# Performance work log

Measured on AMD Instinct MI355X. Metric: run time of the kernel, lower is better.

The kernel has to match this reference:

```python
import jax, jax.numpy as jnp
import numpy as np


def setup_inputs() -> dict:
    key = jax.random.key(0)
    k_x, k_w, k_b = jax.random.split(key, 3)
    B, Cin, H, W = 32, 256, 56, 56
    Cout, KH, KW = 256, 3, 3
    x = jax.random.normal(k_x, (B, Cin, H, W), dtype=jnp.float32)
    fp_weight = jax.random.normal(k_w, (Cout, Cin, KH, KW), dtype=jnp.float32)
    # binary quantization, conv_mode='input_ch': per-output-channel scale
    scaling_factors = jnp.mean(jnp.abs(fp_weight), axis=(1, 2, 3), keepdims=True)  # [Cout,1,1,1]
    quant_weights = jnp.sign(fp_weight)  # values in {-1,0,1}
    bias = jax.random.normal(k_b, (Cout,), dtype=jnp.float32)
    return {"x": x, "scaling_factors": scaling_factors,
            "quant_weights": quant_weights, "bias": bias}


def reference(x, scaling_factors, quant_weights, bias):
    # Dequantize: per-out-channel scale times sign weights
    new_weights = scaling_factors * quant_weights  # [Cout,Cin,3,3]
    out = jax.lax.conv_general_dilated(
        x, new_weights,
        window_strides=(1, 1),
        padding=((1, 1), (1, 1)),
        dimension_numbers=("NCHW", "OIHW", "NCHW"),
    )
    return out + bias[None, :, None, None]
```

## Files before the change

kernel.cpp:

```cpp
#include <hip/hip_runtime.h>

using half8   = __attribute__((ext_vector_type(8))) _Float16;
using floatx4 = __attribute__((ext_vector_type(4))) float;
using floatx2 = __attribute__((ext_vector_type(2))) float;
using short8  = __attribute__((ext_vector_type(8))) short;

__global__ void repack_weights(const float* __restrict__ qw,
                               _Float16* __restrict__ wre, int n) {
  int t = blockIdx.x * 256 + threadIdx.x;
  if (t >= n) return;
  int c = t & 255, co = (t >> 8) & 255, s = t >> 16;
  wre[t] = (_Float16)qw[(co * 256 + c) * 9 + s];
}

__global__ __launch_bounds__(512, 4) void binconv_fused(
    const float* __restrict__ x, const float* __restrict__ scale,
    const float* __restrict__ bias, const _Float16* __restrict__ wre,
    float* __restrict__ out)
{
  __shared__ _Float16 xs[2 * 4 * 64 * 40];

  const int tid  = threadIdx.x;
  const int nb   = blockIdx.x;
  const int b    = nb / 28;
  const int h0   = (nb % 28) * 2;
  const int wave = tid >> 6;
  const int lane = tid & 63;
  const int nl   = lane & 15;
  const int quad = lane >> 4;
  const int co_wave = wave * 32;

  {
    short8 z = {0, 0, 0, 0, 0, 0, 0, 0};
    short8* xs8 = reinterpret_cast<short8*>(xs);
#pragma unroll
    for (int i = 0; i < 5; ++i) xs8[tid + i * 512] = z;
  }

  const int r     = wave >> 1;
  const int chalf = wave & 1;
  const int sc    = lane & 15;
  const int q     = lane >> 4;
  const int ch    = chalf * 16 + sc;
  const int w0    = q * 14;
  const int h     = h0 + r - 1;
  const bool hok  = (h >= 0) && (h < 56);
  const float* xc = x + (((size_t)b * 256 + ch) * 56 + (hok ? h : 0)) * 56 + w0;
  _Float16* const wrow = xs + r * 2560 + ch;

  floatx2 va[7];

  int bbase[7];
#pragma unroll
  for (int j = 0; j < 7; ++j) {
    int n = j * 16 + nl;
    int rr = (n >= 56) ? 1 : 0;
    int w = n - rr * 56;
    bbase[j] = (rr * 64 + w) * 80 + quad * 16;
  }

  const _Float16* aptr[2];
#pragma unroll
  for (int mi = 0; mi < 2; ++mi)
    aptr[mi] = wre + (co_wave + mi * 16 + nl) * 256 + quad * 8;

  floatx4 acc[2][7];
#pragma unroll
  for (int mi = 0; mi < 2; ++mi)
#pragma unroll
    for (int j = 0; j < 7; ++j)
      acc[mi][j] = (floatx4){0.f, 0.f, 0.f, 0.f};

  __syncthreads();

  if (hok) {
#pragma unroll
    for (int i = 0; i < 7; ++i)
      va[i] = *reinterpret_cast<const floatx2*>(xc + 2 * i);
#pragma unroll
    for (int i = 0; i < 7; ++i) {
      wrow[(w0 + 2 * i + 1) * 40] = (_Float16)va[i][0];
      wrow[(w0 + 2 * i + 2) * 40] = (_Float16)va[i][1];
    }
  }

  int bufe = 0;
  for (int cc = 0; cc < 8; ++cc) {
    __syncthreads();
    if (cc < 7 && hok) {
      const float* A = xc + (size_t)(cc + 1) * 100352;
#pragma unroll
      for (int i = 0; i < 7; ++i)
        va[i] = *reinterpret_cast<const floatx2*>(A + 2 * i);
    }
    const int c0 = cc * 32;
    const char* xb = reinterpret_cast<const char*>(xs) + bufe * 2;
    __builtin_amdgcn_s_setprio(1);
#pragma unroll
    for (int s = 0; s < 9; ++s) {
      const int kh = s / 3, kw = s - kh * 3;
      half8 a[2];
#pragma unroll
      for (int mi = 0; mi < 2; ++mi)
        a[mi] = *reinterpret_cast<const half8*>(aptr[mi] + s * 65536 + c0);
      const int soff = (kh * 64 + kw) * 80;
#pragma unroll
      for (int j = 0; j < 7; ++j) {
        half8 bf = *reinterpret_cast<const half8*>(xb + bbase[j] + soff);
#pragma unroll
        for (int mi = 0; mi < 2; ++mi)
          acc[mi][j] = __builtin_amdgcn_mfma_f32_16x16x32_f16(a[mi], bf, acc[mi][j], 0, 0, 0);
      }
    }
    __builtin_amdgcn_s_setprio(0);
    if (cc < 7 && hok) {
      _Float16* d = wrow + (bufe ^ 10240);
#pragma unroll
      for (int i = 0; i < 7; ++i) {
        d[(w0 + 2 * i + 1) * 40] = (_Float16)va[i][0];
        d[(w0 + 2 * i + 2) * 40] = (_Float16)va[i][1];
      }
    }
    bufe ^= 10240;
  }

#pragma unroll
  for (int mi = 0; mi < 2; ++mi) {
#pragma unroll
    for (int reg = 0; reg < 4; ++reg) {
      int co = co_wave + mi * 16 + quad * 4 + reg;
      float s_ = scale[co];
      float bi = bias[co];
#pragma unroll
      for (int j = 0; j < 7; ++j) {
        int n = j * 16 + nl;
        int rr = (n >= 56) ? 1 : 0;
        int w = n - rr * 56;
        out[(((size_t)b * 256 + co) * 56 + (h0 + rr)) * 56 + w] =
            acc[mi][j][reg] * s_ + bi;
      }
    }
  }
}

extern "C" void kernel_launch(void* const* d_in, const int* in_sizes, int n_in,
                              void* d_out, int out_size, void* d_ws, size_t ws_size,
                              hipStream_t stream) {
  const float* x     = (const float*)d_in[0];
  const float* scale = (const float*)d_in[1];
  const float* qw    = (const float*)d_in[2];
  const float* bias  = (const float*)d_in[3];
  float* out = (float*)d_out;

  _Float16* wre = (_Float16*)d_ws;

  repack_weights<<<2304, 256, 0, stream>>>(qw, wre, 9 * 256 * 256);
  binconv_fused<<<896, 512, 0, stream>>>(x, scale, bias, wre, out);
}
```

Baseline: 323.0 us.

## Pre-transpose input to padded fp16 layout and stream it into LDS with direct loads

```diff
diff --git a/kernel.cpp b/kernel.cpp
--- a/kernel.cpp
+++ b/kernel.cpp
@@ -4,6 +4,155 @@
 using floatx4 = __attribute__((ext_vector_type(4))) float;
 using floatx2 = __attribute__((ext_vector_type(2))) float;
 using short8  = __attribute__((ext_vector_type(8))) short;
+
+#define XT_ROW_ELEMS 2560
+#define XT_ROW_BYTES 5120
+#define XT_OFF ((size_t)2 << 20)
+#define XT_BYTES ((size_t)256 * 58 * XT_ROW_BYTES)
+
+__device__ __forceinline__ void dma16(const void* g, void* l) {
+  __builtin_amdgcn_global_load_lds(
+      (const __attribute__((address_space(1))) void*)g,
+      (__attribute__((address_space(3))) void*)l, 16, 0, 0);
+}
+
+__global__ __launch_bounds__(256) void prep_kernel(
+    const float* __restrict__ x, const float* __restrict__ qw,
+    _Float16* __restrict__ wre, _Float16* __restrict__ xt)
+{
+  const int bid = blockIdx.x;
+  const int t = threadIdx.x;
+  if (bid >= 14848) {
+    int idx = (bid - 14848) * 256 + t;
+    int c = idx & 255, co = (idx >> 8) & 255, s = idx >> 16;
+    wre[idx] = (_Float16)qw[(co * 256 + c) * 9 + s];
+    return;
+  }
+  __shared__ _Float16 lt[32 * 57];
+  const int hh = bid % 58;
+  const int bc = bid / 58;
+  const int cc = bc & 7, b = bc >> 3;
+  _Float16* dst = xt + ((size_t)bc * 58 + hh) * XT_ROW_ELEMS;
+  const bool interior = (hh >= 1) && (hh <= 56);
+  if (interior) {
+    const int c = t >> 3, j = t & 7;
+    const float* src = x + (((size_t)(b * 256 + cc * 32 + c)) * 56 + (hh - 1)) * 56 + j * 7;
+#pragma unroll
+    for (int i = 0; i < 7; ++i) lt[c * 57 + j * 7 + i] = (_Float16)src[i];
+  }
+  __syncthreads();
+  for (int ch = t; ch < 320; ch += 256) {
+    int pos = ch / 5, sl = ch - pos * 5;
+    short8 v = {0, 0, 0, 0, 0, 0, 0, 0};
+    if (interior && sl < 4 && pos >= 1 && pos <= 56) {
+      int w = pos - 1;
+#pragma unroll
+      for (int i = 0; i < 8; ++i)
+        v[i] = __builtin_bit_cast(short, lt[(sl * 8 + i) * 57 + w]);
+    }
+    *reinterpret_cast<short8*>(dst + ch * 8) = v;
+  }
+}
+
+__global__ __launch_bounds__(256, 4) void binconv_v3(
+    const float* __restrict__ scale, const float* __restrict__ bias,
+    const _Float16* __restrict__ wre, const _Float16* __restrict__ xt,
+    float* __restrict__ out)
+{
+  __shared__ _Float16 xs[2 * 4 * 64 * 40];
+
+  const int tid    = threadIdx.x;
+  const int bid    = blockIdx.x;
+  const int cohalf = bid & 1;
+  const int nb     = bid >> 1;
+  const int b      = nb / 28;
+  const int h0     = (nb % 28) * 2;
+  const int wave   = tid >> 6;
+  const int lane   = tid & 63;
+  const int nl     = lane & 15;
+  const int quad   = lane >> 4;
+  const int co_wave = cohalf * 128 + wave * 32;
+
+  int bbase[7];
+#pragma unroll
+  for (int j = 0; j < 7; ++j) {
+    int n = j * 16 + nl;
+    int r = (n >= 56) ? 1 : 0;
+    int w = n - r * 56;
+    bbase[j] = (r * 64 + w) * 80 + quad * 16;
+  }
+
+  const _Float16* aptr[2];
+#pragma unroll
+  for (int mi = 0; mi < 2; ++mi)
+    aptr[mi] = wre + (co_wave + mi * 16 + nl) * 256 + quad * 8;
+
+  floatx4 acc[2][7];
+#pragma unroll
+  for (int mi = 0; mi < 2; ++mi)
+#pragma unroll
+    for (int j = 0; j < 7; ++j)
+      acc[mi][j] = (floatx4){0.f, 0.f, 0.f, 0.f};
+
+  const char* xsrc = (const char*)(xt + ((size_t)(b * 8) * 58 + h0) * XT_ROW_ELEMS);
+  const int wlane = wave * XT_ROW_BYTES + lane * 16;
+  const int wldso = wave * XT_ROW_BYTES;
+
+#pragma unroll
+  for (int i = 0; i < 5; ++i)
+    dma16(xsrc + wlane + i * 1024, (char*)xs + wldso + i * 1024);
+
+  int bufoff = 0;
+  for (int cc = 0; cc < 8; ++cc) {
+    __syncthreads();
+    if (cc < 7) {
+      const char* srcn = xsrc + (size_t)(cc + 1) * (58 * XT_ROW_BYTES);
+#pragma unroll
+      for (int i = 0; i < 5; ++i)
+        dma16(srcn + wlane + i * 1024,
+              (char*)xs + (bufoff ^ 20480) + wldso + i * 1024);
+    }
+    const int c0 = cc * 32;
+    const char* xb = (const char*)xs + bufoff;
+    __builtin_amdgcn_s_setprio(1);
+#pragma unroll
+    for (int s = 0; s < 9; ++s) {
+      const int kh = s / 3, kw = s - kh * 3;
+      half8 a[2];
+#pragma unroll
+      for (int mi = 0; mi < 2; ++mi)
+        a[mi] = *reinterpret_cast<const half8*>(aptr[mi] + s * 65536 + c0);
+      const int soff = (kh * 64 + kw) * 80;
+#pragma unroll
+      for (int j = 0; j < 7; ++j) {
+        half8 bf = *reinterpret_cast<const half8*>(xb + bbase[j] + soff);
+#pragma unroll
+        for (int mi = 0; mi < 2; ++mi)
+          acc[mi][j] = __builtin_amdgcn_mfma_f32_16x16x32_f16(a[mi], bf, acc[mi][j], 0, 0, 0);
+      }
+    }
+    __builtin_amdgcn_s_setprio(0);
+    bufoff ^= 20480;
+  }
+
+#pragma unroll
+  for (int mi = 0; mi < 2; ++mi) {
+#pragma unroll
+    for (int reg = 0; reg < 4; ++reg) {
+      int co = co_wave + mi * 16 + quad * 4 + reg;
+      float s_ = scale[co];
+      float bi = bias[co];
+#pragma unroll
+      for (int j = 0; j < 7; ++j) {
+        int n = j * 16 + nl;
+        int r = (n >= 56) ? 1 : 0;
+        int w = n - r * 56;
+        out[(((size_t)b * 256 + co) * 56 + (h0 + r)) * 56 + w] =
+            acc[mi][j][reg] * s_ + bi;
+      }
+    }
+  }
+}
 
 __global__ void repack_weights(const float* __restrict__ qw,
                                _Float16* __restrict__ wre, int n) {
@@ -19,7 +168,6 @@
     float* __restrict__ out)
 {
   __shared__ _Float16 xs[2 * 4 * 64 * 40];
-
   const int tid  = threadIdx.x;
   const int nb   = blockIdx.x;
   const int b    = nb / 28;
@@ -29,14 +177,12 @@
   const int nl   = lane & 15;
   const int quad = lane >> 4;
   const int co_wave = wave * 32;
-
   {
     short8 z = {0, 0, 0, 0, 0, 0, 0, 0};
     short8* xs8 = reinterpret_cast<short8*>(xs);
 #pragma unroll
     for (int i = 0; i < 5; ++i) xs8[tid + i * 512] = z;
   }
-
   const int r     = wave >> 1;
   const int chalf = wave & 1;
   const int sc    = lane & 15;
@@ -47,9 +193,7 @@
   const bool hok  = (h >= 0) && (h < 56);
   const float* xc = x + (((size_t)b * 256 + ch) * 56 + (hok ? h : 0)) * 56 + w0;
   _Float16* const wrow = xs + r * 2560 + ch;
-
   floatx2 va[7];
-
   int bbase[7];
 #pragma unroll
   for (int j = 0; j < 7; ++j) {
@@ -58,21 +202,17 @@
     int w = n - rr * 56;
     bbase[j] = (rr * 64 + w) * 80 + quad * 16;
   }
-
   const _Float16* aptr[2];
 #pragma unroll
   for (int mi = 0; mi < 2; ++mi)
     aptr[mi] = wre + (co_wave + mi * 16 + nl) * 256 + quad * 8;
-
   floatx4 acc[2][7];
 #pragma unroll
   for (int mi = 0; mi < 2; ++mi)
 #pragma unroll
     for (int j = 0; j < 7; ++j)
       acc[mi][j] = (floatx4){0.f, 0.f, 0.f, 0.f};
-
   __syncthreads();
-
   if (hok) {
 #pragma unroll
     for (int i = 0; i < 7; ++i)
@@ -83,7 +223,6 @@
       wrow[(w0 + 2 * i + 2) * 40] = (_Float16)va[i][1];
     }
   }
-
   int bufe = 0;
   for (int cc = 0; cc < 8; ++cc) {
     __syncthreads();
@@ -95,7 +234,6 @@
     }
     const int c0 = cc * 32;
     const char* xb = reinterpret_cast<const char*>(xs) + bufe * 2;
-    __builtin_amdgcn_s_setprio(1);
 #pragma unroll
     for (int s = 0; s < 9; ++s) {
       const int kh = s / 3, kw = s - kh * 3;
@@ -112,7 +250,6 @@
           acc[mi][j] = __builtin_amdgcn_mfma_f32_16x16x32_f16(a[mi], bf, acc[mi][j], 0, 0, 0);
       }
     }
-    __builtin_amdgcn_s_setprio(0);
     if (cc < 7 && hok) {
       _Float16* d = wrow + (bufe ^ 10240);
 #pragma unroll
@@ -123,7 +260,6 @@
     }
     bufe ^= 10240;
   }
-
 #pragma unroll
   for (int mi = 0; mi < 2; ++mi) {
 #pragma unroll
@@ -154,6 +290,12 @@
 
   _Float16* wre = (_Float16*)d_ws;
 
-  repack_weights<<<2304, 256, 0, stream>>>(qw, wre, 9 * 256 * 256);
-  binconv_fused<<<896, 512, 0, stream>>>(x, scale, bias, wre, out);
-}
+  if (ws_size >= XT_OFF + XT_BYTES) {
+    _Float16* xt = (_Float16*)((char*)d_ws + XT_OFF);
+    prep_kernel<<<17152, 256, 0, stream>>>(x, qw, wre, xt);
+    binconv_v3<<<1792, 256, 0, stream>>>(scale, bias, wre, xt, out);
+  } else {
+    repack_weights<<<2304, 256, 0, stream>>>(qw, wre, 9 * 256 * 256);
+    binconv_fused<<<896, 512, 0, stream>>>(x, scale, bias, wre, out);
+  }
+}
```

New measurement: 341.2 us. 1.06x slower.
